# Performance work log

Measured on AMD Instinct MI355X. Metric: run time of the kernel, lower is better.

Reference implementation:

```python
import jax, jax.numpy as jnp
import numpy as np

HEADS = 8
DIM_HEAD = 64
SCALE = DIM_HEAD ** (-0.5)


def setup_inputs() -> dict:
    key = jax.random.key(0)
    k1, k2, k3, k4 = jax.random.split(key, 4)
    B, H, W, n, dim = 2, 64, 64, 8, 512
    inner = HEADS * DIM_HEAD  # 512
    x = jax.random.normal(k1, (B, H, W, n, dim), dtype=jnp.float32)
    mask = jax.random.uniform(k2, (B, H, W, 1, n, n), dtype=jnp.float32)
    w_qkv = jax.random.normal(k3, (dim, 3 * inner), dtype=jnp.float32) * 0.02
    w_out = jax.random.normal(k4, (inner, dim), dtype=jnp.float32) * 0.02
    b_out = jnp.zeros((dim,), dtype=jnp.float32)
    return {"x": x, "mask": mask, "w_qkv": w_qkv, "w_out": w_out, "b_out": b_out}


def reference(x, mask, w_qkv, w_out, b_out):
    B, H, W, n, dim = x.shape
    inner = HEADS * DIM_HEAD
    qkv = x @ w_qkv  # [B,H,W,n,3*inner]
    q, k, v = jnp.split(qkv, 3, axis=-1)

    def to_heads(t):
        # 'B H W n (h d) -> B H W h n d'
        t = t.reshape(B, H, W, n, HEADS, DIM_HEAD)
        return jnp.swapaxes(t, 3, 4)

    q, k, v = to_heads(q), to_heads(k), to_heads(v)
    dots = jnp.einsum('bxyhnd,bxyhmd->bxyhnm', q, k) * SCALE
    dots = dots * mask  # multiplicative mask pre-softmax
    attn = jax.nn.softmax(dots, axis=-1)
    out = jnp.einsum('bxyhnm,bxyhmd->bxyhnd', attn, v)
    # 'B H W h n d -> B H W n (h d)'
    out = jnp.swapaxes(out, 3, 4).reshape(B, H, W, n, inner)
    return out @ w_out + b_out
```

## Files before the change

kernel.cpp:

```cpp
#include <hip/hip_runtime.h>
#include <hip/hip_bf16.h>

#define NROWS 65536
#define DIM   512
#define SCALE_ 0.125f

typedef short bf16x8 __attribute__((ext_vector_type(8)));
typedef unsigned short u16x8 __attribute__((ext_vector_type(8)));
typedef float f32x4 __attribute__((ext_vector_type(4)));

__device__ __forceinline__ unsigned short f2bf(float f) {
  union { float f; unsigned u; } v; v.f = f;
  unsigned r = v.u + 0x7FFFu + ((v.u >> 16) & 1u);
  return (unsigned short)(r >> 16);
}

#define GLL16(gptr, lptr) \
  __builtin_amdgcn_global_load_lds((const __attribute__((address_space(1))) void*)(gptr), \
                                   (__attribute__((address_space(3))) void*)(lptr), 16, 0, 0)

__global__ void prep_kernel(const float* __restrict__ x,
                            const float* __restrict__ wqkv,
                            const float* __restrict__ wout,
                            unsigned short* __restrict__ xb,
                            unsigned short* __restrict__ wqkvT,
                            unsigned short* __restrict__ woutT) {
  if (blockIdx.x < 16384) {
    size_t i = ((size_t)blockIdx.x * 256 + threadIdx.x) * 8;
    float4 a = *(const float4*)(x + i);
    float4 b = *(const float4*)(x + i + 4);
    u16x8 p;
    p[0] = f2bf(a.x); p[1] = f2bf(a.y); p[2] = f2bf(a.z); p[3] = f2bf(a.w);
    p[4] = f2bf(b.x); p[5] = f2bf(b.y); p[6] = f2bf(b.z); p[7] = f2bf(b.w);
    *(u16x8*)(xb + i) = p;
  } else {
    int idx = (blockIdx.x - 16384) * 256 + threadIdx.x;
    if (idx < 1536 * 512) {
      int j = idx >> 9, c = idx & 511;
      wqkvT[idx] = f2bf(wqkv[(size_t)c * 1536 + j]);
    } else {
      int k2 = idx - 1536 * 512;
      int n = k2 >> 9, c = k2 & 511;
      woutT[k2] = f2bf(wout[(size_t)c * 512 + n]);
    }
  }
}

__global__ __launch_bounds__(256, 2)
void qkv_attn_kernel(const unsigned short* __restrict__ xb,
                     const float* __restrict__ mask,
                     const unsigned short* __restrict__ wqkvT,
                     unsigned short* __restrict__ attn_out) {
  __shared__ __align__(16) unsigned char smem[81920];

  const int t = threadIdx.x;
  const int lane = t & 63, wave = t >> 6;
  const int wm = wave >> 1, wn = wave & 1;
  const int fr = lane & 15, fq = lane >> 4;
  const int swz = (((lane & 3) ^ ((lane >> 2) & 3))) * 8;

  const int per = gridDim.x >> 3;
  const int lin = (blockIdx.x & 7) * per + (blockIdx.x >> 3);
  const int mtile = lin >> 3, head = lin & 7;
  const int r0 = mtile * 128;

  f32x4 acc[4][6];
  const f32x4 z4 = {0.f, 0.f, 0.f, 0.f};
  #pragma unroll
  for (int m = 0; m < 4; ++m)
    #pragma unroll
    for (int n = 0; n < 6; ++n) acc[m][n] = z4;

  auto STAGE = [&](int buf, int kt2) {
    unsigned char* base = smem + buf * 20480;
    const int k0 = kt2 * 32;
    #pragma unroll
    for (int i = 0; i < 2; ++i) {
      int c = wave * 2 + i;
      const unsigned short* g =
          xb + (size_t)(r0 + c * 16 + (lane >> 2)) * 512 + k0 + swz;
      GLL16(g, base + c * 1024);
    }
    #pragma unroll
    for (int i = 0; i < 3; ++i) {
      int c = wave * 3 + i;
      int n = c * 16 + (lane >> 2);
      int jg = ((n >> 6) << 9) + head * 64 + (n & 63);
      GLL16(wqkvT + (size_t)jg * 512 + k0 + swz, base + 8192 + c * 1024);
    }
  };

  auto COMPUTE = [&](int buf) {
    unsigned char* Ab = smem + buf * 20480;
    unsigned char* Bb = Ab + 8192;
    const unsigned ko = ((unsigned)(fq ^ (fr & 3))) << 4;
    bf16x8 a[4], b[6];
    #pragma unroll
    for (int m = 0; m < 4; ++m)
      a[m] = *(const bf16x8*)(Ab + (unsigned)(wm * 64 + m * 16 + fr) * 64 + ko);
    #pragma unroll
    for (int n = 0; n < 6; ++n)
      b[n] = *(const bf16x8*)(Bb + (unsigned)(wn * 96 + n * 16 + fr) * 64 + ko);
    #pragma unroll
    for (int m = 0; m < 4; ++m)
      #pragma unroll
      for (int n = 0; n < 6; ++n)
        acc[m][n] = __builtin_amdgcn_mfma_f32_16x16x32_bf16(a[m], b[n], acc[m][n], 0, 0, 0);
  };

  STAGE(0, 0);
  STAGE(1, 1);
  for (int kt = 0; kt < 14; ++kt) {
    STAGE((kt + 2) & 3, kt + 2);
    asm volatile("s_waitcnt vmcnt(10)" ::: "memory");
    __builtin_amdgcn_s_barrier();
    COMPUTE(kt & 3);
  }
  asm volatile("s_waitcnt vmcnt(5)" ::: "memory");
  __builtin_amdgcn_s_barrier();
  COMPUTE(2);
  asm volatile("s_waitcnt vmcnt(0)" ::: "memory");
  __builtin_amdgcn_s_barrier();
  COMPUTE(3);
  __syncthreads();

  unsigned short* Qs = (unsigned short*)smem;
  unsigned short* Ks = (unsigned short*)(smem + 16384);
  unsigned short* VT = (unsigned short*)(smem + 32768);
  unsigned short* Pl = (unsigned short*)(smem + 52224);

  float mreg[2][4];
  #pragma unroll
  for (int pp = 0; pp < 2; ++pp) {
    int pair = wave * 2 + pp;
    #pragma unroll
    for (int r = 0; r < 4; ++r) {
      int row = fq * 4 + r;
      int Pg = mtile * 16 + pair * 2 + (row >> 3);
      mreg[pp][r] = mask[(size_t)Pg * 64 + (row & 7) * 8 + (fr & 7)];
    }
  }

  {
    int d = t >> 2, q = t & 3;
    ushort4 z; z.x = 0; z.y = 0; z.z = 0; z.w = 0;
    *(ushort4*)(VT + d * 152 + 128 + q * 4) = z;
  }
  #pragma unroll
  for (int n = 0; n < 6; ++n) {
    int col = wn * 96 + n * 16 + fr;
    #pragma unroll
    for (int m = 0; m < 4; ++m) {
      if (col < 128) {
        unsigned short* T = (col < 64) ? Qs : Ks;
        unsigned cc = (unsigned)(col & 63);
        #pragma unroll
        for (int r = 0; r < 4; ++r) {
          int row = wm * 64 + m * 16 + fq * 4 + r;
          unsigned byte = (unsigned)row * 128 + ((cc * 2) ^ (((unsigned)(row & 7)) << 4));
          *(unsigned short*)((unsigned char*)T + byte) = f2bf(acc[m][n][r]);
        }
      } else {
        int d = col - 128;
        ushort4 p;
        p.x = f2bf(acc[m][n][0]); p.y = f2bf(acc[m][n][1]);
        p.z = f2bf(acc[m][n][2]); p.w = f2bf(acc[m][n][3]);
        *(ushort4*)(VT + d * 152 + (wm * 64 + m * 16 + fq * 4)) = p;
      }
    }
  }
  __syncthreads();

  #pragma unroll
  for (int pp = 0; pp < 2; ++pp) {
    const int pair = wave * 2 + pp;
    const unsigned rbyte = (unsigned)(pair * 16 + fr) * 128;
    const unsigned xrp = ((unsigned)(fr & 7)) << 4;
    f32x4 s = {0.f, 0.f, 0.f, 0.f};
    #pragma unroll
    for (int kk = 0; kk < 2; ++kk) {
      const unsigned ko = ((unsigned)(kk * 64 + fq * 16)) ^ xrp;
      bf16x8 qf = *(const bf16x8*)((unsigned char*)Qs + rbyte + ko);
      bf16x8 kf = *(const bf16x8*)((unsigned char*)Ks + rbyte + ko);
      s = __builtin_amdgcn_mfma_f32_16x16x32_bf16(qf, kf, s, 0, 0, 0);
    }
    float p4[4];
    #pragma unroll
    for (int r = 0; r < 4; ++r) {
      int row = fq * 4 + r;
      bool valid = (row >> 3) == (fr >> 3);
      p4[r] = valid ? s[r] * SCALE_ * mreg[pp][r] : -3.0e38f;
    }
    #pragma unroll
    for (int r = 0; r < 4; ++r) {
      float v = p4[r];
      float mx = v;
      mx = fmaxf(mx, __shfl_xor(mx, 1));
      mx = fmaxf(mx, __shfl_xor(mx, 2));
      mx = fmaxf(mx, __shfl_xor(mx, 4));
      float e = __expf(v - mx);
      float sm = e;
      sm += __shfl_xor(sm, 1);
      sm += __shfl_xor(sm, 2);
      sm += __shfl_xor(sm, 4);
      p4[r] = e / sm;
    }
    #pragma unroll
    for (int r = 0; r < 4; ++r) {
      int row = fq * 4 + r;
      bool valid = (row >> 3) == (fr >> 3);
      Pl[pair * 640 + row * 40 + fr] = valid ? f2bf(p4[r]) : (unsigned short)0;
      Pl[pair * 640 + row * 40 + 16 + fr] = 0;
    }
    #pragma unroll
    for (int dblk = 0; dblk < 4; ++dblk) {
      bf16x8 af = *(const bf16x8*)((unsigned char*)VT +
                    (unsigned)(dblk * 16 + fr) * 304 + (unsigned)(pair * 32 + fq * 16));
      bf16x8 bf = *(const bf16x8*)((unsigned char*)Pl +
                    (unsigned)pair * 1280 + (unsigned)fr * 80 + (unsigned)fq * 16);
      f32x4 o = {0.f, 0.f, 0.f, 0.f};
      o = __builtin_amdgcn_mfma_f32_16x16x32_bf16(af, bf, o, 0, 0, 0);
      ushort4 pk;
      pk.x = f2bf(o[0]); pk.y = f2bf(o[1]); pk.z = f2bf(o[2]); pk.w = f2bf(o[3]);
      *(ushort4*)(attn_out + (size_t)(r0 + pair * 16 + fr) * 512 +
                  head * 64 + dblk * 16 + fq * 4) = pk;
    }
  }
}

__global__ __launch_bounds__(256, 2)
void outproj_kernel(const unsigned short* __restrict__ attn,
                    const unsigned short* __restrict__ woutT,
                    const float* __restrict__ bias,
                    float* __restrict__ out) {
  __shared__ __align__(16) unsigned char smem[65536];
  const int t = threadIdx.x;
  const int lane = t & 63, wave = t >> 6;
  const int wm = wave >> 1, wn = wave & 1;
  const int fr = lane & 15, fq = lane >> 4;
  const int l8 = lane >> 3;
  const int cswz = ((lane & 7) ^ l8) * 8;

  const int per = gridDim.x >> 3;
  const int lin = (blockIdx.x & 7) * per + (blockIdx.x >> 3);
  const int mtile = lin >> 2, nt = lin & 3;
  const int r0 = mtile * 128, n0 = nt * 128;

  f32x4 acc[4][4];
  const f32x4 z4 = {0.f, 0.f, 0.f, 0.f};
  #pragma unroll
  for (int m = 0; m < 4; ++m)
    #pragma unroll
    for (int n = 0; n < 4; ++n) acc[m][n] = z4;

  auto STAGE = [&](int buf, int kt2) {
    unsigned char* base = smem + buf * 32768;
    const int k0 = kt2 * 64;
    const unsigned short* gA = attn  + (size_t)(r0 + l8) * 512 + k0 + cswz;
    const unsigned short* gB = woutT + (size_t)(n0 + l8) * 512 + k0 + cswz;
    #pragma unroll
    for (int i = 0; i < 4; ++i) {
      int c = wave * 4 + i;
      GLL16(gA + (size_t)c * 8 * 512, base + c * 1024);
      GLL16(gB + (size_t)c * 8 * 512, base + 16384 + c * 1024);
    }
  };

  STAGE(0, 0);
  asm volatile("s_waitcnt vmcnt(0)" ::: "memory");
  __syncthreads();
  int cur = 0;

  for (int kt = 0; kt < 8; ++kt) {
    if (kt < 7) STAGE(cur ^ 1, kt + 1);
    unsigned char* Ab = smem + cur * 32768;
    unsigned char* Bb = Ab + 16384;
    const unsigned xr = ((unsigned)(fr & 7)) << 4;
    #pragma unroll
    for (int kk = 0; kk < 2; ++kk) {
      const unsigned ko = ((unsigned)(kk * 64 + fq * 16)) ^ xr;
      bf16x8 a[4], b[4];
      #pragma unroll
      for (int m = 0; m < 4; ++m)
        a[m] = *(const bf16x8*)(Ab + (unsigned)(wm * 64 + m * 16 + fr) * 128 + ko);
      #pragma unroll
      for (int n = 0; n < 4; ++n)
        b[n] = *(const bf16x8*)(Bb + (unsigned)(wn * 64 + n * 16 + fr) * 128 + ko);
      #pragma unroll
      for (int m = 0; m < 4; ++m)
        #pragma unroll
        for (int n = 0; n < 4; ++n)
          acc[m][n] = __builtin_amdgcn_mfma_f32_16x16x32_bf16(a[m], b[n], acc[m][n], 0, 0, 0);
    }
    asm volatile("s_waitcnt vmcnt(0)" ::: "memory");
    __syncthreads();
    cur ^= 1;
  }
  #pragma unroll
  for (int n = 0; n < 4; ++n) {
    int col = n0 + wn * 64 + n * 16 + fr;
    float bv = bias[col];
    #pragma unroll
    for (int m = 0; m < 4; ++m) {
      #pragma unroll
      for (int j = 0; j < 4; ++j) {
        int row = r0 + wm * 64 + m * 16 + fq * 4 + j;
        out[(size_t)row * 512 + col] = acc[m][n][j] + bv;
      }
    }
  }
}

extern "C" void kernel_launch(void* const* d_in, const int* in_sizes, int n_in,
                              void* d_out, int out_size, void* d_ws, size_t ws_size,
                              hipStream_t stream) {
  const float* x    = (const float*)d_in[0];
  const float* mask = (const float*)d_in[1];
  const float* wqkv = (const float*)d_in[2];
  const float* wout = (const float*)d_in[3];
  const float* bias = (const float*)d_in[4];
  float* out = (float*)d_out;

  unsigned char* ws = (unsigned char*)d_ws;
  unsigned short* attn  = (unsigned short*)ws;
  unsigned short* wqkvT = (unsigned short*)(ws + 67108864);
  unsigned short* woutT = (unsigned short*)(ws + 67108864 + 1572864);
  unsigned short* xb    = (unsigned short*)(ws + 67108864 + 1572864 + 524288);

  prep_kernel<<<20480, 256, 0, stream>>>(x, wqkv, wout, xb, wqkvT, woutT);
  qkv_attn_kernel<<<4096, 256, 0, stream>>>(xb, mask, wqkvT, attn);
  outproj_kernel<<<2048, 256, 0, stream>>>(attn, woutT, bias, out);
}
```

Before: 235.2 us.

## Process two heads per block with 8 waves and phased ping-pong QKV pipeline

The QKV+attention kernel now uses 512-thread blocks that each compute two heads for a 128-row tile. This halves the number of blocks and lets the X tile be loaded once and reused across both heads. The GEMM main loop is restructured into a double-buffered pipeline with K=64 steps, split into four phases that interleave LDS reads, async global-to-LDS loads, barriers and priority-raised MFMA bursts. LDS use rises to 128KB per block and the extra barriers may reduce occupancy, and the wait counts must be correct for the new load sequencing.

```diff
diff --git a/kernel.cpp b/kernel.cpp
--- a/kernel.cpp
+++ b/kernel.cpp
@@ -18,6 +18,8 @@
 #define GLL16(gptr, lptr) \
   __builtin_amdgcn_global_load_lds((const __attribute__((address_space(1))) void*)(gptr), \
                                    (__attribute__((address_space(3))) void*)(lptr), 16, 0, 0)
+#define VMCNT(n) asm volatile("s_waitcnt vmcnt(" #n ")" ::: "memory")
+#define LGKM0   asm volatile("s_waitcnt lgkmcnt(0)" ::: "memory")
 
 __global__ void prep_kernel(const float* __restrict__ x,
                             const float* __restrict__ wqkv,
@@ -46,23 +48,26 @@
   }
 }
 
-__global__ __launch_bounds__(256, 2)
+__global__ __launch_bounds__(512, 2)
 void qkv_attn_kernel(const unsigned short* __restrict__ xb,
                      const float* __restrict__ mask,
                      const unsigned short* __restrict__ wqkvT,
                      unsigned short* __restrict__ attn_out) {
-  __shared__ __align__(16) unsigned char smem[81920];
+  __shared__ __align__(16) unsigned char smem[131072];
 
   const int t = threadIdx.x;
-  const int lane = t & 63, wave = t >> 6;
-  const int wm = wave >> 1, wn = wave & 1;
+  const int lane = t & 63, w = t >> 6;
+  const int wm = w >> 2, wn = w & 3;
   const int fr = lane & 15, fq = lane >> 4;
-  const int swz = (((lane & 3) ^ ((lane >> 2) & 3))) * 8;
+  const int l4 = lane >> 2, ls = lane & 3;
+  const int sigma = (ls ^ (l4 & 3)) * 8;
+  const unsigned rko = ((unsigned)(fq ^ (fr & 3))) << 4;
 
   const int per = gridDim.x >> 3;
   const int lin = (blockIdx.x & 7) * per + (blockIdx.x >> 3);
-  const int mtile = lin >> 3, head = lin & 7;
+  const int mtile = lin >> 2, hp = lin & 3;
   const int r0 = mtile * 128;
+  const int head0 = hp * 2;
 
   f32x4 acc[4][6];
   const f32x4 z4 = {0.f, 0.f, 0.f, 0.f};
@@ -71,68 +76,103 @@
     #pragma unroll
     for (int n = 0; n < 6; ++n) acc[m][n] = z4;
 
-  auto STAGE = [&](int buf, int kt2) {
-    unsigned char* base = smem + buf * 20480;
-    const int k0 = kt2 * 32;
-    #pragma unroll
-    for (int i = 0; i < 2; ++i) {
-      int c = wave * 2 + i;
-      const unsigned short* g =
-          xb + (size_t)(r0 + c * 16 + (lane >> 2)) * 512 + k0 + swz;
-      GLL16(g, base + c * 1024);
-    }
-    #pragma unroll
-    for (int i = 0; i < 3; ++i) {
-      int c = wave * 3 + i;
-      int n = c * 16 + (lane >> 2);
-      int jg = ((n >> 6) << 9) + head * 64 + (n & 63);
-      GLL16(wqkvT + (size_t)jg * 512 + k0 + swz, base + 8192 + c * 1024);
-    }
-  };
-
-  auto COMPUTE = [&](int buf) {
-    unsigned char* Ab = smem + buf * 20480;
-    unsigned char* Bb = Ab + 8192;
-    const unsigned ko = ((unsigned)(fq ^ (fr & 3))) << 4;
-    bf16x8 a[4], b[6];
+  auto STAGE_A = [&](int buf, int kt2, int kh) {
+    unsigned char* dst = smem + buf * 65536 + kh * 8192 + w * 1024;
+    const unsigned short* g =
+        xb + (size_t)(r0 + w * 16 + l4) * 512 + kt2 * 64 + kh * 32 + sigma;
+    GLL16(g, dst);
+  };
+  auto STAGE_B = [&](int buf, int kt2, int kh, int i) {
+    int n = (w * 3 + i) * 16 + l4;
+    int g = n >> 7, hh = (n >> 6) & 1, j = n & 63;
+    unsigned char* dst = smem + buf * 65536 + 16384 + kh * 24576 + (w * 3 + i) * 1024;
+    const unsigned short* src =
+        wqkvT + (size_t)((g << 9) + (head0 + hh) * 64 + j) * 512 + kt2 * 64 + kh * 32 + sigma;
+    GLL16(src, dst);
+  };
+
+  auto RD_A = [&](int buf, int kh, bf16x8* a) {
+    unsigned char* base = smem + buf * 65536 + kh * 8192;
     #pragma unroll
     for (int m = 0; m < 4; ++m)
-      a[m] = *(const bf16x8*)(Ab + (unsigned)(wm * 64 + m * 16 + fr) * 64 + ko);
-    #pragma unroll
-    for (int n = 0; n < 6; ++n)
-      b[n] = *(const bf16x8*)(Bb + (unsigned)(wn * 96 + n * 16 + fr) * 64 + ko);
+      a[m] = *(const bf16x8*)(base + (unsigned)(wm * 64 + m * 16 + fr) * 64 + rko);
+  };
+  auto RD_B = [&](int buf, int kh, int nh, bf16x8* b) {
+    unsigned char* base = smem + buf * 65536 + 16384 + kh * 24576;
+    #pragma unroll
+    for (int i = 0; i < 3; ++i)
+      b[i] = *(const bf16x8*)(base + (unsigned)(wn * 96 + (nh * 3 + i) * 16 + fr) * 64 + rko);
+  };
+  auto MFMA12 = [&](bf16x8* a, bf16x8* b, int nh) {
     #pragma unroll
     for (int m = 0; m < 4; ++m)
       #pragma unroll
-      for (int n = 0; n < 6; ++n)
-        acc[m][n] = __builtin_amdgcn_mfma_f32_16x16x32_bf16(a[m], b[n], acc[m][n], 0, 0, 0);
-  };
-
-  STAGE(0, 0);
-  STAGE(1, 1);
-  for (int kt = 0; kt < 14; ++kt) {
-    STAGE((kt + 2) & 3, kt + 2);
-    asm volatile("s_waitcnt vmcnt(10)" ::: "memory");
-    __builtin_amdgcn_s_barrier();
-    COMPUTE(kt & 3);
-  }
-  asm volatile("s_waitcnt vmcnt(5)" ::: "memory");
-  __builtin_amdgcn_s_barrier();
-  COMPUTE(2);
-  asm volatile("s_waitcnt vmcnt(0)" ::: "memory");
-  __builtin_amdgcn_s_barrier();
-  COMPUTE(3);
+      for (int i = 0; i < 3; ++i)
+        acc[m][nh * 3 + i] =
+            __builtin_amdgcn_mfma_f32_16x16x32_bf16(a[m], b[i], acc[m][nh * 3 + i], 0, 0, 0);
+  };
+
+  STAGE_A(0, 0, 0); STAGE_B(0, 0, 0, 0); STAGE_B(0, 0, 0, 1); STAGE_B(0, 0, 0, 2);
+  STAGE_A(0, 0, 1); STAGE_B(0, 0, 1, 0); STAGE_B(0, 0, 1, 1); STAGE_B(0, 0, 1, 2);
+  VMCNT(4);
   __syncthreads();
 
-  unsigned short* Qs = (unsigned short*)smem;
-  unsigned short* Ks = (unsigned short*)(smem + 16384);
-  unsigned short* VT = (unsigned short*)(smem + 32768);
-  unsigned short* Pl = (unsigned short*)(smem + 52224);
-
+  for (int kt = 0; kt < 8; ++kt) {
+    const int cur = kt & 1, nxt = cur ^ 1;
+    const bool stg = (kt < 7);
+    bf16x8 a[4], b[3];
+
+    RD_A(cur, 0, a); RD_B(cur, 0, 0, b);
+    if (stg) { STAGE_A(nxt, kt + 1, 0); STAGE_B(nxt, kt + 1, 0, 0); }
+    __builtin_amdgcn_s_barrier();
+    LGKM0; __builtin_amdgcn_sched_barrier(0);
+    __builtin_amdgcn_s_setprio(1);
+    MFMA12(a, b, 0);
+    __builtin_amdgcn_s_setprio(0);
+    __builtin_amdgcn_s_barrier();
+
+    RD_B(cur, 0, 1, b);
+    if (stg) {
+      STAGE_B(nxt, kt + 1, 0, 1); STAGE_B(nxt, kt + 1, 0, 2);
+      VMCNT(4);
+    } else {
+      VMCNT(0);
+    }
+    __builtin_amdgcn_s_barrier();
+    LGKM0; __builtin_amdgcn_sched_barrier(0);
+    __builtin_amdgcn_s_setprio(1);
+    MFMA12(a, b, 1);
+    __builtin_amdgcn_s_setprio(0);
+    __builtin_amdgcn_s_barrier();
+
+    RD_A(cur, 1, a); RD_B(cur, 1, 0, b);
+    if (stg) { STAGE_A(nxt, kt + 1, 1); STAGE_B(nxt, kt + 1, 1, 0); }
+    __builtin_amdgcn_s_barrier();
+    LGKM0; __builtin_amdgcn_sched_barrier(0);
+    __builtin_amdgcn_s_setprio(1);
+    MFMA12(a, b, 0);
+    __builtin_amdgcn_s_setprio(0);
+    __builtin_amdgcn_s_barrier();
+
+    RD_B(cur, 1, 1, b);
+    if (stg) {
+      STAGE_B(nxt, kt + 1, 1, 1); STAGE_B(nxt, kt + 1, 1, 2);
+      VMCNT(4);
+    }
+    __builtin_amdgcn_s_barrier();
+    LGKM0; __builtin_amdgcn_sched_barrier(0);
+    __builtin_amdgcn_s_setprio(1);
+    MFMA12(a, b, 1);
+    __builtin_amdgcn_s_setprio(0);
+    __builtin_amdgcn_s_barrier();
+  }
+
+
+  const int hh_w = w >> 2, pq = w & 3;
   float mreg[2][4];
   #pragma unroll
   for (int pp = 0; pp < 2; ++pp) {
-    int pair = wave * 2 + pp;
+    int pair = pq * 2 + pp;
     #pragma unroll
     for (int r = 0; r < 4; ++r) {
       int row = fq * 4 + r;
@@ -142,38 +182,44 @@
   }
 
   {
-    int d = t >> 2, q = t & 3;
+    int zh = t >> 8, d = (t >> 2) & 63, q = t & 3;
     ushort4 z; z.x = 0; z.y = 0; z.z = 0; z.w = 0;
-    *(ushort4*)(VT + d * 152 + 128 + q * 4) = z;
+    *(ushort4*)(smem + zh * 52224 + 32768 + d * 304 + 256 + q * 8) = z;
   }
   #pragma unroll
   for (int n = 0; n < 6; ++n) {
     int col = wn * 96 + n * 16 + fr;
+    int g = col >> 7, hh = (col >> 6) & 1, cc = col & 63;
+    unsigned char* hb = smem + hh * 52224;
     #pragma unroll
     for (int m = 0; m < 4; ++m) {
-      if (col < 128) {
-        unsigned short* T = (col < 64) ? Qs : Ks;
-        unsigned cc = (unsigned)(col & 63);
+      if (g == 2) {
+        ushort4 p;
+        p.x = f2bf(acc[m][n][0]); p.y = f2bf(acc[m][n][1]);
+        p.z = f2bf(acc[m][n][2]); p.w = f2bf(acc[m][n][3]);
+        *(ushort4*)(hb + 32768 + cc * 304 + (unsigned)(wm * 64 + m * 16 + fq * 4) * 2) = p;
+      } else {
+        unsigned char* T = hb + g * 16384;
         #pragma unroll
         for (int r = 0; r < 4; ++r) {
           int row = wm * 64 + m * 16 + fq * 4 + r;
-          unsigned byte = (unsigned)row * 128 + ((cc * 2) ^ (((unsigned)(row & 7)) << 4));
-          *(unsigned short*)((unsigned char*)T + byte) = f2bf(acc[m][n][r]);
+          unsigned byte = (unsigned)row * 128 + (((unsigned)cc * 2) ^ (((unsigned)(row & 7)) << 4));
+          *(unsigned short*)(T + byte) = f2bf(acc[m][n][r]);
         }
-      } else {
-        int d = col - 128;
-        ushort4 p;
-        p.x = f2bf(acc[m][n][0]); p.y = f2bf(acc[m][n][1]);
-        p.z = f2bf(acc[m][n][2]); p.w = f2bf(acc[m][n][3]);
-        *(ushort4*)(VT + d * 152 + (wm * 64 + m * 16 + fq * 4)) = p;
       }
     }
   }
   __syncthreads();
 
+  unsigned char* hb = smem + hh_w * 52224;
+  unsigned short* Qs = (unsigned short*)hb;
+  unsigned short* Ks = (unsigned short*)(hb + 16384);
+  unsigned char*  VTb = hb + 32768;
+
   #pragma unroll
   for (int pp = 0; pp < 2; ++pp) {
-    const int pair = wave * 2 + pp;
+    const int pair = pq * 2 + pp;
+    unsigned short* Pl = (unsigned short*)(smem + 104448) + (hh_w * 8 + pair) * 640;
     const unsigned rbyte = (unsigned)(pair * 16 + fr) * 128;
     const unsigned xrp = ((unsigned)(fr & 7)) << 4;
     f32x4 s = {0.f, 0.f, 0.f, 0.f};
@@ -209,21 +255,21 @@
     for (int r = 0; r < 4; ++r) {
       int row = fq * 4 + r;
       bool valid = (row >> 3) == (fr >> 3);
-      Pl[pair * 640 + row * 40 + fr] = valid ? f2bf(p4[r]) : (unsigned short)0;
-      Pl[pair * 640 + row * 40 + 16 + fr] = 0;
+      Pl[row * 40 + fr] = valid ? f2bf(p4[r]) : (unsigned short)0;
+      Pl[row * 40 + 16 + fr] = 0;
     }
     #pragma unroll
     for (int dblk = 0; dblk < 4; ++dblk) {
-      bf16x8 af = *(const bf16x8*)((unsigned char*)VT +
+      bf16x8 af = *(const bf16x8*)(VTb +
                     (unsigned)(dblk * 16 + fr) * 304 + (unsigned)(pair * 32 + fq * 16));
       bf16x8 bf = *(const bf16x8*)((unsigned char*)Pl +
-                    (unsigned)pair * 1280 + (unsigned)fr * 80 + (unsigned)fq * 16);
+                    (unsigned)fr * 80 + (unsigned)fq * 16);
       f32x4 o = {0.f, 0.f, 0.f, 0.f};
       o = __builtin_amdgcn_mfma_f32_16x16x32_bf16(af, bf, o, 0, 0, 0);
       ushort4 pk;
       pk.x = f2bf(o[0]); pk.y = f2bf(o[1]); pk.z = f2bf(o[2]); pk.w = f2bf(o[3]);
       *(ushort4*)(attn_out + (size_t)(r0 + pair * 16 + fr) * 512 +
-                  head * 64 + dblk * 16 + fq * 4) = pk;
+                  (head0 + hh_w) * 64 + dblk * 16 + fq * 4) = pk;
     }
   }
 }
@@ -267,7 +313,7 @@
   };
 
   STAGE(0, 0);
-  asm volatile("s_waitcnt vmcnt(0)" ::: "memory");
+  VMCNT(0);
   __syncthreads();
   int cur = 0;
 
@@ -292,7 +338,7 @@
         for (int n = 0; n < 4; ++n)
           acc[m][n] = __builtin_amdgcn_mfma_f32_16x16x32_bf16(a[m], b[n], acc[m][n], 0, 0, 0);
     }
-    asm volatile("s_waitcnt vmcnt(0)" ::: "memory");
+    VMCNT(0);
     __syncthreads();
     cur ^= 1;
   }
@@ -328,6 +374,6 @@
   unsigned short* xb    = (unsigned short*)(ws + 67108864 + 1572864 + 524288);
 
   prep_kernel<<<20480, 256, 0, stream>>>(x, wqkv, wout, xb, wqkvT, woutT);
-  qkv_attn_kernel<<<4096, 256, 0, stream>>>(xb, mask, wqkvT, attn);
+  qkv_attn_kernel<<<2048, 512, 0, stream>>>(xb, mask, wqkvT, attn);
   outproj_kernel<<<2048, 256, 0, stream>>>(attn, woutT, bias, out);
 }
```

Result: slower. 248.4 us (+5.6%).

## Restructure QKV-attention kernel for per-wave row ownership and higher occupancy

Applied to the files above, without the earlier changes.

The QKV projection kernel is reorganized so each wave owns 32 rows across all 192 columns (Q, K, V for one head). This lets the attention stage run entirely in per-wave LDS regions with no block-wide barriers. Shared memory shrinks from 80KB to 40KB by using a two-stage double buffer instead of four stages, and launch bounds go to 4 blocks per CU to raise occupancy. The change also adds s_setprio around the MFMA groups and a new LDS swizzle. In exchange, the shallower prefetch with a full vmcnt(0) wait each iteration exposes more load latency, and each wave now reloads the full B tile from LDS.

```diff
diff --git a/kernel.cpp b/kernel.cpp
--- a/kernel.cpp
+++ b/kernel.cpp
@@ -18,6 +18,8 @@
 #define GLL16(gptr, lptr) \
   __builtin_amdgcn_global_load_lds((const __attribute__((address_space(1))) void*)(gptr), \
                                    (__attribute__((address_space(3))) void*)(lptr), 16, 0, 0)
+#define VMCNT(n) asm volatile("s_waitcnt vmcnt(" #n ")" ::: "memory")
+#define LGKM0    asm volatile("s_waitcnt lgkmcnt(0)" ::: "memory")
 
 __global__ void prep_kernel(const float* __restrict__ x,
                             const float* __restrict__ wqkv,
@@ -46,137 +48,121 @@
   }
 }
 
-__global__ __launch_bounds__(256, 2)
+__global__ __launch_bounds__(256, 4)
 void qkv_attn_kernel(const unsigned short* __restrict__ xb,
                      const float* __restrict__ mask,
                      const unsigned short* __restrict__ wqkvT,
                      unsigned short* __restrict__ attn_out) {
-  __shared__ __align__(16) unsigned char smem[81920];
+  __shared__ __align__(16) unsigned char smem[40960];
 
   const int t = threadIdx.x;
-  const int lane = t & 63, wave = t >> 6;
-  const int wm = wave >> 1, wn = wave & 1;
+  const int lane = t & 63, w = t >> 6;
   const int fr = lane & 15, fq = lane >> 4;
-  const int swz = (((lane & 3) ^ ((lane >> 2) & 3))) * 8;
+  const int l4 = lane >> 2, ls = lane & 3;
+  const int sigma = ((ls ^ (l4 ^ (l4 >> 2))) & 3) * 8;
+  const unsigned rko = ((unsigned)(fq ^ ((fr ^ (fr >> 2)) & 3))) << 4;
 
   const int per = gridDim.x >> 3;
   const int lin = (blockIdx.x & 7) * per + (blockIdx.x >> 3);
   const int mtile = lin >> 3, head = lin & 7;
   const int r0 = mtile * 128;
 
-  f32x4 acc[4][6];
+  f32x4 acc[2][12];
   const f32x4 z4 = {0.f, 0.f, 0.f, 0.f};
   #pragma unroll
-  for (int m = 0; m < 4; ++m)
-    #pragma unroll
-    for (int n = 0; n < 6; ++n) acc[m][n] = z4;
+  for (int m = 0; m < 2; ++m)
+    #pragma unroll
+    for (int n = 0; n < 12; ++n) acc[m][n] = z4;
 
   auto STAGE = [&](int buf, int kt2) {
     unsigned char* base = smem + buf * 20480;
     const int k0 = kt2 * 32;
     #pragma unroll
     for (int i = 0; i < 2; ++i) {
-      int c = wave * 2 + i;
-      const unsigned short* g =
-          xb + (size_t)(r0 + c * 16 + (lane >> 2)) * 512 + k0 + swz;
-      GLL16(g, base + c * 1024);
+      int c = w * 2 + i;
+      GLL16(xb + (size_t)(r0 + c * 16 + l4) * 512 + k0 + sigma, base + c * 1024);
     }
     #pragma unroll
     for (int i = 0; i < 3; ++i) {
-      int c = wave * 3 + i;
-      int n = c * 16 + (lane >> 2);
+      int c = w * 3 + i;
+      int n = c * 16 + l4;
       int jg = ((n >> 6) << 9) + head * 64 + (n & 63);
-      GLL16(wqkvT + (size_t)jg * 512 + k0 + swz, base + 8192 + c * 1024);
+      GLL16(wqkvT + (size_t)jg * 512 + k0 + sigma, base + 8192 + c * 1024);
     }
   };
 
   auto COMPUTE = [&](int buf) {
     unsigned char* Ab = smem + buf * 20480;
     unsigned char* Bb = Ab + 8192;
-    const unsigned ko = ((unsigned)(fq ^ (fr & 3))) << 4;
-    bf16x8 a[4], b[6];
-    #pragma unroll
-    for (int m = 0; m < 4; ++m)
-      a[m] = *(const bf16x8*)(Ab + (unsigned)(wm * 64 + m * 16 + fr) * 64 + ko);
-    #pragma unroll
-    for (int n = 0; n < 6; ++n)
-      b[n] = *(const bf16x8*)(Bb + (unsigned)(wn * 96 + n * 16 + fr) * 64 + ko);
-    #pragma unroll
-    for (int m = 0; m < 4; ++m)
-      #pragma unroll
-      for (int n = 0; n < 6; ++n)
-        acc[m][n] = __builtin_amdgcn_mfma_f32_16x16x32_bf16(a[m], b[n], acc[m][n], 0, 0, 0);
+    bf16x8 a[2];
+    #pragma unroll
+    for (int m = 0; m < 2; ++m)
+      a[m] = *(const bf16x8*)(Ab + (unsigned)(w * 32 + m * 16 + fr) * 64 + rko);
+    #pragma unroll
+    for (int nh = 0; nh < 4; ++nh) {
+      bf16x8 b[3];
+      #pragma unroll
+      for (int i = 0; i < 3; ++i)
+        b[i] = *(const bf16x8*)(Bb + (unsigned)((nh * 3 + i) * 16 + fr) * 64 + rko);
+      __builtin_amdgcn_s_setprio(1);
+      #pragma unroll
+      for (int m = 0; m < 2; ++m)
+        #pragma unroll
+        for (int i = 0; i < 3; ++i)
+          acc[m][nh * 3 + i] =
+              __builtin_amdgcn_mfma_f32_16x16x32_bf16(a[m], b[i], acc[m][nh * 3 + i], 0, 0, 0);
+      __builtin_amdgcn_s_setprio(0);
+    }
   };
 
   STAGE(0, 0);
-  STAGE(1, 1);
-  for (int kt = 0; kt < 14; ++kt) {
-    STAGE((kt + 2) & 3, kt + 2);
-    asm volatile("s_waitcnt vmcnt(10)" ::: "memory");
-    __builtin_amdgcn_s_barrier();
-    COMPUTE(kt & 3);
-  }
-  asm volatile("s_waitcnt vmcnt(5)" ::: "memory");
-  __builtin_amdgcn_s_barrier();
-  COMPUTE(2);
-  asm volatile("s_waitcnt vmcnt(0)" ::: "memory");
-  __builtin_amdgcn_s_barrier();
-  COMPUTE(3);
+  VMCNT(0);
   __syncthreads();
-
-  unsigned short* Qs = (unsigned short*)smem;
-  unsigned short* Ks = (unsigned short*)(smem + 16384);
-  unsigned short* VT = (unsigned short*)(smem + 32768);
-  unsigned short* Pl = (unsigned short*)(smem + 52224);
+  for (int kt = 0; kt < 16; ++kt) {
+    if (kt < 15) STAGE((kt + 1) & 1, kt + 1);
+    COMPUTE(kt & 1);
+    VMCNT(0);
+    __syncthreads();
+  }
+
+  unsigned char* wreg = smem + w * 10240;
+  unsigned short* Qs = (unsigned short*)wreg;
+  unsigned short* Ks = (unsigned short*)(wreg + 4096);
 
   float mreg[2][4];
   #pragma unroll
-  for (int pp = 0; pp < 2; ++pp) {
-    int pair = wave * 2 + pp;
+  for (int pr = 0; pr < 2; ++pr) {
     #pragma unroll
     for (int r = 0; r < 4; ++r) {
-      int row = fq * 4 + r;
-      int Pg = mtile * 16 + pair * 2 + (row >> 3);
-      mreg[pp][r] = mask[(size_t)Pg * 64 + (row & 7) * 8 + (fr & 7)];
-    }
-  }
-
-  {
-    int d = t >> 2, q = t & 3;
-    ushort4 z; z.x = 0; z.y = 0; z.z = 0; z.w = 0;
-    *(ushort4*)(VT + d * 152 + 128 + q * 4) = z;
-  }
-  #pragma unroll
-  for (int n = 0; n < 6; ++n) {
-    int col = wn * 96 + n * 16 + fr;
-    #pragma unroll
-    for (int m = 0; m < 4; ++m) {
-      if (col < 128) {
-        unsigned short* T = (col < 64) ? Qs : Ks;
-        unsigned cc = (unsigned)(col & 63);
-        #pragma unroll
-        for (int r = 0; r < 4; ++r) {
-          int row = wm * 64 + m * 16 + fq * 4 + r;
-          unsigned byte = (unsigned)row * 128 + ((cc * 2) ^ (((unsigned)(row & 7)) << 4));
-          *(unsigned short*)((unsigned char*)T + byte) = f2bf(acc[m][n][r]);
-        }
-      } else {
-        int d = col - 128;
-        ushort4 p;
-        p.x = f2bf(acc[m][n][0]); p.y = f2bf(acc[m][n][1]);
-        p.z = f2bf(acc[m][n][2]); p.w = f2bf(acc[m][n][3]);
-        *(ushort4*)(VT + d * 152 + (wm * 64 + m * 16 + fq * 4)) = p;
+      int q = fq * 4 + r;
+      int Pg = mtile * 16 + w * 4 + pr * 2 + (q >> 3);
+      mreg[pr][r] = mask[(size_t)Pg * 64 + (q & 7) * 8 + (fr & 7)];
+    }
+  }
+
+  #pragma unroll
+  for (int n = 0; n < 8; ++n) {
+    int col = n * 16 + fr;
+    unsigned short* T = (n < 4) ? Qs : Ks;
+    unsigned cc = (unsigned)(col & 63);
+    #pragma unroll
+    for (int m = 0; m < 2; ++m) {
+      #pragma unroll
+      for (int r = 0; r < 4; ++r) {
+        int lr = m * 16 + fq * 4 + r;
+        unsigned byte = (unsigned)lr * 128 + ((cc * 2) ^ (((unsigned)(lr & 7)) << 4));
+        *(unsigned short*)((unsigned char*)T + byte) = f2bf(acc[m][n][r]);
       }
     }
   }
-  __syncthreads();
-
-  #pragma unroll
-  for (int pp = 0; pp < 2; ++pp) {
-    const int pair = wave * 2 + pp;
-    const unsigned rbyte = (unsigned)(pair * 16 + fr) * 128;
+  LGKM0; __builtin_amdgcn_sched_barrier(0);
+
+  f32x4 s2[2];
+  #pragma unroll
+  for (int pr = 0; pr < 2; ++pr) {
+    const unsigned rbyte = (unsigned)(pr * 16 + fr) * 128;
     const unsigned xrp = ((unsigned)(fr & 7)) << 4;
-    f32x4 s = {0.f, 0.f, 0.f, 0.f};
+    f32x4 s = z4;
     #pragma unroll
     for (int kk = 0; kk < 2; ++kk) {
       const unsigned ko = ((unsigned)(kk * 64 + fq * 16)) ^ xrp;
@@ -184,16 +170,17 @@
       bf16x8 kf = *(const bf16x8*)((unsigned char*)Ks + rbyte + ko);
       s = __builtin_amdgcn_mfma_f32_16x16x32_bf16(qf, kf, s, 0, 0, 0);
     }
-    float p4[4];
+    s2[pr] = s;
+  }
+
+  float p4[2][4];
+  #pragma unroll
+  for (int pr = 0; pr < 2; ++pr) {
     #pragma unroll
     for (int r = 0; r < 4; ++r) {
-      int row = fq * 4 + r;
-      bool valid = (row >> 3) == (fr >> 3);
-      p4[r] = valid ? s[r] * SCALE_ * mreg[pp][r] : -3.0e38f;
-    }
-    #pragma unroll
-    for (int r = 0; r < 4; ++r) {
-      float v = p4[r];
+      int q = fq * 4 + r;
+      bool valid = (q >> 3) == (fr >> 3);
+      float v = valid ? s2[pr][r] * SCALE_ * mreg[pr][r] : -3.0e38f;
       float mx = v;
       mx = fmaxf(mx, __shfl_xor(mx, 1));
       mx = fmaxf(mx, __shfl_xor(mx, 2));
@@ -203,26 +190,49 @@
       sm += __shfl_xor(sm, 1);
       sm += __shfl_xor(sm, 2);
       sm += __shfl_xor(sm, 4);
-      p4[r] = e / sm;
-    }
+      p4[pr][r] = e / sm;
+    }
+  }
+  asm volatile("" ::: "memory");
+
+  unsigned short* VT = (unsigned short*)wreg;
+  #pragma unroll
+  for (int n = 8; n < 12; ++n) {
+    int d = (n - 8) * 16 + fr;
+    #pragma unroll
+    for (int m = 0; m < 2; ++m) {
+      ushort4 p;
+      p.x = f2bf(acc[m][n][0]); p.y = f2bf(acc[m][n][1]);
+      p.z = f2bf(acc[m][n][2]); p.w = f2bf(acc[m][n][3]);
+      *(ushort4*)(VT + d * 40 + m * 16 + fq * 4) = p;
+    }
+  }
+  #pragma unroll
+  for (int pr = 0; pr < 2; ++pr) {
+    unsigned short* Pl = (unsigned short*)(wreg + 5120 + pr * 1280);
     #pragma unroll
     for (int r = 0; r < 4; ++r) {
-      int row = fq * 4 + r;
-      bool valid = (row >> 3) == (fr >> 3);
-      Pl[pair * 640 + row * 40 + fr] = valid ? f2bf(p4[r]) : (unsigned short)0;
-      Pl[pair * 640 + row * 40 + 16 + fr] = 0;
-    }
+      int q = fq * 4 + r;
+      bool valid = (q >> 3) == (fr >> 3);
+      Pl[q * 40 + pr * 16 + fr] = valid ? f2bf(p4[pr][r]) : (unsigned short)0;
+      Pl[q * 40 + (1 - pr) * 16 + fr] = 0;
+    }
+  }
+  LGKM0; __builtin_amdgcn_sched_barrier(0);
+
+  #pragma unroll
+  for (int pr = 0; pr < 2; ++pr) {
+    unsigned char* Plb = wreg + 5120 + pr * 1280;
     #pragma unroll
     for (int dblk = 0; dblk < 4; ++dblk) {
       bf16x8 af = *(const bf16x8*)((unsigned char*)VT +
-                    (unsigned)(dblk * 16 + fr) * 304 + (unsigned)(pair * 32 + fq * 16));
-      bf16x8 bf = *(const bf16x8*)((unsigned char*)Pl +
-                    (unsigned)pair * 1280 + (unsigned)fr * 80 + (unsigned)fq * 16);
+                    (unsigned)(dblk * 16 + fr) * 80 + (unsigned)fq * 16);
+      bf16x8 bf = *(const bf16x8*)(Plb + (unsigned)fr * 80 + (unsigned)fq * 16);
       f32x4 o = {0.f, 0.f, 0.f, 0.f};
       o = __builtin_amdgcn_mfma_f32_16x16x32_bf16(af, bf, o, 0, 0, 0);
       ushort4 pk;
       pk.x = f2bf(o[0]); pk.y = f2bf(o[1]); pk.z = f2bf(o[2]); pk.w = f2bf(o[3]);
-      *(ushort4*)(attn_out + (size_t)(r0 + pair * 16 + fr) * 512 +
+      *(ushort4*)(attn_out + (size_t)(r0 + w * 32 + pr * 16 + fr) * 512 +
                   head * 64 + dblk * 16 + fq * 4) = pk;
     }
   }
@@ -267,7 +277,7 @@
   };
 
   STAGE(0, 0);
-  asm volatile("s_waitcnt vmcnt(0)" ::: "memory");
+  VMCNT(0);
   __syncthreads();
   int cur = 0;
 
@@ -292,7 +302,7 @@
         for (int n = 0; n < 4; ++n)
           acc[m][n] = __builtin_amdgcn_mfma_f32_16x16x32_bf16(a[m], b[n], acc[m][n], 0, 0, 0);
     }
-    asm volatile("s_waitcnt vmcnt(0)" ::: "memory");
+    VMCNT(0);
     __syncthreads();
     cur ^= 1;
   }
```

Result: slower. 256.0 us (+8.8%).

## Load QKV GEMM A operand directly to registers, double-buffer B in LDS

Applied to the files above, without the earlier changes.

In the fused QKV+attention kernel, the x tile is now loaded straight from global memory into registers (double-buffered across k-steps) instead of staged through LDS. Only the weight tile goes through LDS, with a wider 64-wide k-step, a new XOR swizzle and 2 buffers instead of 4. This cuts LDS traffic and shrinks shared memory from 80KB to 61KB, which may allow more blocks per CU. In exchange it raises register pressure (16 extra bf16x8 operand registers), adds an extra barrier per iteration, and has waves in the same row redundantly loading the same A rows from global memory.

```diff
diff --git a/kernel.cpp b/kernel.cpp
--- a/kernel.cpp
+++ b/kernel.cpp
@@ -18,6 +18,8 @@
 #define GLL16(gptr, lptr) \
   __builtin_amdgcn_global_load_lds((const __attribute__((address_space(1))) void*)(gptr), \
                                    (__attribute__((address_space(3))) void*)(lptr), 16, 0, 0)
+#define VMCNT(n) asm volatile("s_waitcnt vmcnt(" #n ")" ::: "memory")
+#define LGKM0    asm volatile("s_waitcnt lgkmcnt(0)" ::: "memory")
 
 __global__ void prep_kernel(const float* __restrict__ x,
                             const float* __restrict__ wqkv,
@@ -51,13 +53,14 @@
                      const float* __restrict__ mask,
                      const unsigned short* __restrict__ wqkvT,
                      unsigned short* __restrict__ attn_out) {
-  __shared__ __align__(16) unsigned char smem[81920];
+  __shared__ __align__(16) unsigned char smem[62464];
 
   const int t = threadIdx.x;
   const int lane = t & 63, wave = t >> 6;
   const int wm = wave >> 1, wn = wave & 1;
   const int fr = lane & 15, fq = lane >> 4;
-  const int swz = (((lane & 3) ^ ((lane >> 2) & 3))) * 8;
+  const int l8 = lane >> 3;
+  const int cswz = ((lane & 7) ^ l8) * 8;
 
   const int per = gridDim.x >> 3;
   const int lin = (blockIdx.x & 7) * per + (blockIdx.x >> 3);
@@ -71,58 +74,60 @@
     #pragma unroll
     for (int n = 0; n < 6; ++n) acc[m][n] = z4;
 
-  auto STAGE = [&](int buf, int kt2) {
-    unsigned char* base = smem + buf * 20480;
-    const int k0 = kt2 * 32;
-    #pragma unroll
-    for (int i = 0; i < 2; ++i) {
-      int c = wave * 2 + i;
-      const unsigned short* g =
-          xb + (size_t)(r0 + c * 16 + (lane >> 2)) * 512 + k0 + swz;
-      GLL16(g, base + c * 1024);
-    }
-    #pragma unroll
-    for (int i = 0; i < 3; ++i) {
-      int c = wave * 3 + i;
-      int n = c * 16 + (lane >> 2);
+  auto LOAD_A = [&](bf16x8 (&a)[8], int kt2) {
+    const unsigned short* g = xb + (size_t)(r0 + wm * 64 + fr) * 512 + kt2 * 64 + fq * 8;
+    #pragma unroll
+    for (int m = 0; m < 4; ++m)
+      #pragma unroll
+      for (int kk = 0; kk < 2; ++kk)
+        a[m * 2 + kk] = *(const bf16x8*)(g + (size_t)m * 16 * 512 + kk * 32);
+  };
+  auto STAGE_B = [&](int buf, int kt2) {
+    unsigned char* base = smem + buf * 24576;
+    const unsigned short* gB = wqkvT + kt2 * 64 + cswz;
+    #pragma unroll
+    for (int i = 0; i < 6; ++i) {
+      int c = wave * 6 + i;
+      int n = c * 8 + l8;
       int jg = ((n >> 6) << 9) + head * 64 + (n & 63);
-      GLL16(wqkvT + (size_t)jg * 512 + k0 + swz, base + 8192 + c * 1024);
+      GLL16(gB + (size_t)jg * 512, base + c * 1024);
     }
   };
-
-  auto COMPUTE = [&](int buf) {
-    unsigned char* Ab = smem + buf * 20480;
-    unsigned char* Bb = Ab + 8192;
-    const unsigned ko = ((unsigned)(fq ^ (fr & 3))) << 4;
-    bf16x8 a[4], b[6];
-    #pragma unroll
-    for (int m = 0; m < 4; ++m)
-      a[m] = *(const bf16x8*)(Ab + (unsigned)(wm * 64 + m * 16 + fr) * 64 + ko);
-    #pragma unroll
-    for (int n = 0; n < 6; ++n)
-      b[n] = *(const bf16x8*)(Bb + (unsigned)(wn * 96 + n * 16 + fr) * 64 + ko);
-    #pragma unroll
-    for (int m = 0; m < 4; ++m)
+  auto COMPUTE = [&](int buf, bf16x8 (&a)[8]) {
+    unsigned char* Bb = smem + buf * 24576;
+    #pragma unroll
+    for (int kk = 0; kk < 2; ++kk) {
+      const unsigned ko = ((unsigned)(kk * 64 + fq * 16)) ^ (((unsigned)(fr & 7)) << 4);
+      bf16x8 b[6];
       #pragma unroll
       for (int n = 0; n < 6; ++n)
-        acc[m][n] = __builtin_amdgcn_mfma_f32_16x16x32_bf16(a[m], b[n], acc[m][n], 0, 0, 0);
+        b[n] = *(const bf16x8*)(Bb + (unsigned)(wn * 96 + n * 16 + fr) * 128 + ko);
+      #pragma unroll
+      for (int m = 0; m < 4; ++m)
+        #pragma unroll
+        for (int n = 0; n < 6; ++n)
+          acc[m][n] = __builtin_amdgcn_mfma_f32_16x16x32_bf16(a[m * 2 + kk], b[n], acc[m][n], 0, 0, 0);
+    }
   };
 
-  STAGE(0, 0);
-  STAGE(1, 1);
-  for (int kt = 0; kt < 14; ++kt) {
-    STAGE((kt + 2) & 3, kt + 2);
-    asm volatile("s_waitcnt vmcnt(10)" ::: "memory");
+  bf16x8 aA[8], aB[8];
+  LOAD_A(aA, 0);
+  STAGE_B(0, 0);
+  #pragma unroll
+  for (int kt = 0; kt < 8; ++kt) {
+    bf16x8 (&aCur)[8] = (kt & 1) ? aB : aA;
+    bf16x8 (&aNxt)[8] = (kt & 1) ? aA : aB;
+    if (kt < 7) {
+      LOAD_A(aNxt, kt + 1);
+      STAGE_B((kt + 1) & 1, kt + 1);
+      VMCNT(11);
+    } else {
+      VMCNT(0);
+    }
     __builtin_amdgcn_s_barrier();
-    COMPUTE(kt & 3);
-  }
-  asm volatile("s_waitcnt vmcnt(5)" ::: "memory");
-  __builtin_amdgcn_s_barrier();
-  COMPUTE(2);
-  asm volatile("s_waitcnt vmcnt(0)" ::: "memory");
-  __builtin_amdgcn_s_barrier();
-  COMPUTE(3);
-  __syncthreads();
+    COMPUTE(kt & 1, aCur);
+    __builtin_amdgcn_s_barrier();
+  }
 
   unsigned short* Qs = (unsigned short*)smem;
   unsigned short* Ks = (unsigned short*)(smem + 16384);
@@ -267,7 +272,7 @@
   };
 
   STAGE(0, 0);
-  asm volatile("s_waitcnt vmcnt(0)" ::: "memory");
+  VMCNT(0);
   __syncthreads();
   int cur = 0;
 
@@ -292,7 +297,7 @@
         for (int n = 0; n < 4; ++n)
           acc[m][n] = __builtin_amdgcn_mfma_f32_16x16x32_bf16(a[m], b[n], acc[m][n], 0, 0, 0);
     }
-    asm volatile("s_waitcnt vmcnt(0)" ::: "memory");
+    VMCNT(0);
     __syncthreads();
     cur ^= 1;
   }
```

After: 279.8 us. 18.9% more time.
